# Kernel optimization log

Hardware: AMD Instinct MI355X
Metric: run time of the kernel (lower is better)

The kernel has to match this reference:

```python
import jax, jax.numpy as jnp
import numpy as np

B, N, D = 32, 2048, 128
HALF = D // 2
DT = 0.01  # interval = [0.0, 0.01], euler solver -> single step of size 0.01


def setup_inputs() -> dict:
    key = jax.random.key(0)
    ks = jax.random.split(key, 10)
    x = jax.random.normal(ks[0], (B, N, D), dtype=jnp.float32)
    hz = jax.random.normal(ks[1], (B, N, D), dtype=jnp.float32)
    # row-normalized random adjacency so adj @ h stays O(1) (avoids tanh saturation)
    adj = jax.random.uniform(ks[2], (N, N), dtype=jnp.float32) / N
    W1 = jax.random.normal(ks[3], (D, D), dtype=jnp.float32) * 0.05
    W2 = jax.random.normal(ks[4], (D, D), dtype=jnp.float32) * 0.05
    Wa = jax.random.normal(ks[5], (2 * D, 2 * D), dtype=jnp.float32) * 0.05
    ba = jnp.zeros((2 * D,), dtype=jnp.float32)
    Wb = jax.random.normal(ks[6], (2 * D, D), dtype=jnp.float32) * 0.05
    bb = jnp.zeros((D,), dtype=jnp.float32)
    # nn.Parameter init is zeros in torch; randomize in [0,0.1] for a nontrivial baseline
    eps = jax.random.uniform(ks[7], (B, N, HALF), dtype=jnp.float32) * 0.1
    return {"x": x, "hz": hz, "adj": adj, "W1": W1, "W2": W2,
            "Wa": Wa, "ba": ba, "Wb": Wb, "bb": bb, "eps": eps}


def reference(x, hz, adj, W1, W2, Wa, ba, Wb, bb, eps):
    # MLP gating: Linear(2D,2D) -> ReLU -> Linear(2D,D) -> Tanh
    u = jnp.concatenate([x, hz], axis=-1)            # [B,N,2D]
    h = jnp.tanh(jax.nn.relu(u @ Wa + ba) @ Wb + bb)  # [B,N,D]

    def gnn_func(h, W):
        # f(t, h) = tanh(A @ h @ W)  (graph diffusion ODE func)
        return jnp.tanh(jnp.einsum('nm,bmd->bnd', adj, h) @ W)

    def euler_step(h, W):
        # odeint(euler, t=[0, 0.01]): one step y1 = y0 + dt * f(0, y0)
        return h + DT * gnn_func(h, W)

    eps_c = jnp.clip(eps, 0.0, 0.1)
    for _ in range(2):
        h_f = euler_step(h, W1)[..., :HALF]                      # [B,N,D/2]
        h = jnp.concatenate([h_f, h[..., HALF:]], axis=-1)       # [B,N,D]
        h_s = eps_c * euler_step(h, W2)[..., HALF:]              # [B,N,D/2]
        h = jnp.concatenate([h_f, h_s], axis=-1)                 # [B,N,D]
    return h
```

## Files before the change

### kernel.cpp

```cpp
#include <hip/hip_runtime.h>


typedef unsigned short u16;
typedef unsigned int   u32;
typedef unsigned long long u64;
typedef __attribute__((ext_vector_type(8))) short bf8;
typedef __attribute__((ext_vector_type(4))) float f4;

#define AS1 __attribute__((address_space(1)))
#define AS3 __attribute__((address_space(3)))

__device__ __forceinline__ void gl_lds16(const void* g, void* l) {
  __builtin_amdgcn_global_load_lds((const AS1 u32*)g, (AS3 u32*)l, 16, 0, 0);
}
__device__ __forceinline__ float bf2f(u16 v) {
  u32 u = ((u32)v) << 16; return __builtin_bit_cast(float, u);
}
__device__ __forceinline__ u16 f2bf(float f) {
  u32 u = __builtin_bit_cast(u32, f);
  return (u16)((u + 0x7fffu + ((u >> 16) & 1u)) >> 16);
}
__device__ __forceinline__ float ldf(const void* p, size_t i, u32 isf32) {
  return isf32 ? ((const float*)p)[i] : bf2f(((const u16*)p)[i]);
}

__device__ __forceinline__ void stage128x32(const u16* grow0, int stride, u16* lds,
                                            int wave, int lane) {
  int r0 = wave * 16 + (lane >> 2);
  int c0 = (lane & 3) * 8;
  gl_lds16(grow0 + (size_t)r0 * stride + c0, lds + wave * 512);
  gl_lds16(grow0 + (size_t)(64 + r0) * stride + c0, lds + 2048 + wave * 512);
}
__device__ __forceinline__ void stage64x32(const u16* grow0, int stride, u16* lds,
                                           int wave, int lane) {
  gl_lds16(grow0 + (size_t)(wave * 16 + (lane >> 2)) * stride + (lane & 3) * 8,
           lds + wave * 512);
}

__global__ void detect_dtype(const u16* __restrict__ x_raw, u32* __restrict__ flag) {
  __shared__ int s;
  int tid = threadIdx.x;
  if (tid == 0) s = 0;
  __syncthreads();
  int huge = 0;
#pragma unroll
  for (int j = 0; j < 16; ++j) {
    u16 v = x_raw[tid * 16 + j];
    u32 e = (v >> 7) & 0xFF;
    if (e >= 0xC0) huge = 1;
  }
  if (huge) atomicOr(&s, 1);
  __syncthreads();
  if (tid == 0) flag[0] = (u32)s;
}

__global__ void cvt_bf16(const void* __restrict__ in, u16* __restrict__ out,
                         long in_off, int n, const u32* __restrict__ flag) {
  u32 isf32 = flag[0];
  int gid = blockIdx.x * 256 + threadIdx.x;
  long i = in_off + (long)gid * 4;
  if (gid * 4 >= n) return;
  u16 o0, o1, o2, o3;
  if (isf32) {
    f4 v = *(const f4*)&((const float*)in)[i];
    o0 = f2bf(v[0]); o1 = f2bf(v[1]); o2 = f2bf(v[2]); o3 = f2bf(v[3]);
  } else {
    u64 v = *(const u64*)&((const u16*)in)[i];
    o0 = (u16)v; o1 = (u16)(v >> 16); o2 = (u16)(v >> 32); o3 = (u16)(v >> 48);
  }
  u64 pk = (u64)o0 | ((u64)o1 << 16) | ((u64)o2 << 32) | ((u64)o3 << 48);
  *(u64*)&out[(size_t)gid * 4] = pk;
}

__global__ void prep_weights(const void* __restrict__ Wa, const void* __restrict__ Wb,
                             const void* __restrict__ W1, const void* __restrict__ W2,
                             u16* __restrict__ WaT, u16* __restrict__ WbT,
                             u16* __restrict__ W1T, u16* __restrict__ W2T,
                             const u32* __restrict__ flag) {
  u32 isf32 = flag[0];
  int i = blockIdx.x * 256 + threadIdx.x;
  if (i < 65536) {
    int o = i >> 8, k = i & 255; WaT[o * 256 + k] = f2bf(ldf(Wa, (size_t)k * 256 + o, isf32));
  } else if (i < 98304) {
    int j = i - 65536; int o = j >> 8, k = j & 255;
    WbT[o * 256 + k] = f2bf(ldf(Wb, (size_t)k * 128 + o, isf32));
  } else if (i < 106496) {
    int j = i - 98304; int jj = j >> 7, k = j & 127;
    W1T[jj * 128 + k] = f2bf(ldf(W1, (size_t)k * 128 + jj, isf32));
  } else {
    int j = i - 106496; int jj = j >> 7, k = j & 127;
    W2T[jj * 128 + k] = f2bf(ldf(W2, (size_t)k * 128 + 64 + jj, isf32));
  }
}

__global__ __launch_bounds__(256, 2) void mlp_fused(const void* __restrict__ x,
                                                    const void* __restrict__ hz,
                                                    const u16* __restrict__ WaT,
                                                    const void* __restrict__ ba,
                                                    const u16* __restrict__ WbT,
                                                    const void* __restrict__ bb,
                                                    const u16* __restrict__ W1T,
                                                    u16* __restrict__ hT,
                                                    u16* __restrict__ hW,
                                                    const u32* __restrict__ flag) {
  __shared__ __align__(16) u16 Z[64 * 264];
  __shared__ __align__(16) u16 pool[10240];
  u16* lA = pool;
  u16* lB = pool + 2048;
  u16* hN = pool;
  u32 isf32 = flag[0];
  int tid = threadIdx.x, lane = tid & 63, wave = tid >> 6;
  int col = lane & 15, quad = lane >> 4;
  int r0 = blockIdx.x * 64;
  int b = r0 >> 11;

  f4 acc[4][4] = {};
  for (int kk = 0; kk < 8; ++kk) {
    int k0 = kk * 32;
    const void* src = (kk < 4) ? x : hz;
    int csrc = (kk < 4) ? k0 : (k0 - 128);
    __syncthreads();
    {
      int row = tid >> 2, c0 = (tid & 3) * 8;
      size_t g = (size_t)(r0 + row) * 128 + csrc + c0;
      uint4 pk;
      if (isf32) {
        f4 v0 = *(const f4*)&((const float*)src)[g];
        f4 v1 = *(const f4*)&((const float*)src)[g + 4];
        pk.x = (u32)f2bf(v0[0]) | ((u32)f2bf(v0[1]) << 16);
        pk.y = (u32)f2bf(v0[2]) | ((u32)f2bf(v0[3]) << 16);
        pk.z = (u32)f2bf(v1[0]) | ((u32)f2bf(v1[1]) << 16);
        pk.w = (u32)f2bf(v1[2]) | ((u32)f2bf(v1[3]) << 16);
      } else {
        pk = *(const uint4*)&((const u16*)src)[g];
      }
      *(uint4*)&lA[row * 32 + c0] = pk;
    }
    stage128x32(WaT + k0, 256, lB, wave, lane);
    stage128x32(WaT + (size_t)128 * 256 + k0, 256, lB + 4096, wave, lane);
    __syncthreads();
    bf8 af[4], bfr[4];
#pragma unroll
    for (int mi = 0; mi < 4; ++mi) af[mi] = *(const bf8*)&lA[(mi * 16 + col) * 32 + quad * 8];
#pragma unroll
    for (int nj = 0; nj < 4; ++nj) bfr[nj] = *(const bf8*)&lB[(wave * 64 + nj * 16 + col) * 32 + quad * 8];
#pragma unroll
    for (int mi = 0; mi < 4; ++mi)
#pragma unroll
      for (int nj = 0; nj < 4; ++nj)
        acc[mi][nj] = __builtin_amdgcn_mfma_f32_16x16x32_bf16(af[mi], bfr[nj], acc[mi][nj], 0, 0, 0);
  }
#pragma unroll
  for (int mi = 0; mi < 4; ++mi)
#pragma unroll
    for (int nj = 0; nj < 4; ++nj) {
      int o = wave * 64 + nj * 16 + col;
      float bav = ldf(ba, o, isf32);
      int rl = mi * 16 + quad * 4;
#pragma unroll
      for (int r = 0; r < 4; ++r)
        Z[(rl + r) * 264 + o] = f2bf(fmaxf(acc[mi][nj][r] + bav, 0.f));
    }
  __syncthreads();

  f4 acc2[4][2] = {};
  for (int kk = 0; kk < 8; ++kk) {
    int k0 = kk * 32;
    if (kk) __syncthreads();
    stage128x32(WbT + k0, 256, lB, wave, lane);
    __syncthreads();
    bf8 az[4], bw[2];
#pragma unroll
    for (int mi = 0; mi < 4; ++mi) az[mi] = *(const bf8*)&Z[(mi * 16 + col) * 264 + k0 + quad * 8];
#pragma unroll
    for (int nj = 0; nj < 2; ++nj) bw[nj] = *(const bf8*)&lB[(wave * 32 + nj * 16 + col) * 32 + quad * 8];
#pragma unroll
    for (int mi = 0; mi < 4; ++mi)
#pragma unroll
      for (int nj = 0; nj < 2; ++nj)
        acc2[mi][nj] = __builtin_amdgcn_mfma_f32_16x16x32_bf16(az[mi], bw[nj], acc2[mi][nj], 0, 0, 0);
  }
  __syncthreads();

#pragma unroll
  for (int mi = 0; mi < 4; ++mi)
#pragma unroll
    for (int nj = 0; nj < 2; ++nj) {
      int d = wave * 32 + nj * 16 + col;
      float bbv = ldf(bb, d, isf32);
      int rl = mi * 16 + quad * 4;
      int rabs = r0 + rl;
      int n = rabs & 2047;
      u16 p[4];
#pragma unroll
      for (int r = 0; r < 4; ++r) {
        p[r] = f2bf(tanhf(acc2[mi][nj][r] + bbv));
        hN[(rl + r) * 136 + d] = p[r];
      }
      u64 pk = (u64)p[0] | ((u64)p[1] << 16) | ((u64)p[2] << 32) | ((u64)p[3] << 48);
      *(u64*)&hT[(size_t)(b * 128 + d) * 2048 + n] = pk;
    }
  __syncthreads();

  f4 acc3[4] = {};
#pragma unroll
  for (int ks = 0; ks < 4; ++ks) {
    bf8 aw[4], bg;
#pragma unroll
    for (int mi = 0; mi < 4; ++mi)
      aw[mi] = *(const bf8*)&W1T[(size_t)(mi * 16 + col) * 128 + ks * 32 + quad * 8];
    bg = *(const bf8*)&hN[(wave * 16 + col) * 136 + ks * 32 + quad * 8];
#pragma unroll
    for (int mi = 0; mi < 4; ++mi)
      acc3[mi] = __builtin_amdgcn_mfma_f32_16x16x32_bf16(aw[mi], bg, acc3[mi], 0, 0, 0);
  }
#pragma unroll
  for (int mi = 0; mi < 4; ++mi) {
    int rloc = wave * 16 + col;
    int ng = (r0 & 2047) + rloc;
#pragma unroll
    for (int r = 0; r < 4; ++r) {
      int j = mi * 16 + quad * 4 + r;
      hW[(size_t)(b * 64 + j) * 2048 + ng] = f2bf(acc3[mi][r]);
    }
  }
}

__global__ __launch_bounds__(256, 2) void fused_step2(const u16* __restrict__ hin,
                                                      const u16* __restrict__ hWT,
                                                      const u16* __restrict__ adjb,
                                                      const u16* __restrict__ WnT,
                                                      const void* __restrict__ eps,
                                                      u16* __restrict__ hout,
                                                      u16* __restrict__ hWout,
                                                      int half, const u32* __restrict__ flag) {
  __shared__ __align__(16) u16 smem[24576];
  u16* lA = smem;
  u16* lB = smem + 8192;
  u16* gN = smem;
  u32 isf32 = flag[0];
  int tid = threadIdx.x, lane = tid & 63, wave = tid >> 6;
  int col = lane & 15, quad = lane >> 4;
  int b = blockIdx.y;
  int n0 = blockIdx.x * 128;

  const u16* Arow = hWT + (size_t)(b * 64) * 2048;
  const u16* Brow = adjb + (size_t)n0 * 2048;

  f4 acc[4][2] = {};
  for (int kk = 0; kk < 16; ++kk) {
    int k0 = kk * 128;
#pragma unroll
    for (int p = 0; p < 4; ++p) {
      stage64x32(Arow + k0 + p * 32, 2048, lA + p * 2048, wave, lane);
      stage128x32(Brow + k0 + p * 32, 2048, lB + p * 4096, wave, lane);
    }
    __syncthreads();
#pragma unroll
    for (int p = 0; p < 4; ++p) {
      bf8 af[4], bfr[2];
#pragma unroll
      for (int mi = 0; mi < 4; ++mi) af[mi] = *(const bf8*)&lA[p * 2048 + (mi * 16 + col) * 32 + quad * 8];
#pragma unroll
      for (int nj = 0; nj < 2; ++nj) bfr[nj] = *(const bf8*)&lB[p * 4096 + (wave * 32 + nj * 16 + col) * 32 + quad * 8];
#pragma unroll
      for (int mi = 0; mi < 4; ++mi)
#pragma unroll
        for (int nj = 0; nj < 2; ++nj)
          acc[mi][nj] = __builtin_amdgcn_mfma_f32_16x16x32_bf16(af[mi], bfr[nj], acc[mi][nj], 0, 0, 0);
    }
    __syncthreads();
  }

  bool has_eps = (eps != nullptr);
  bool mk_hw = (WnT != nullptr);
  int dBase = half * 64;
#pragma unroll
  for (int mi = 0; mi < 4; ++mi)
#pragma unroll
    for (int nj = 0; nj < 2; ++nj) {
      int j0 = mi * 16 + quad * 4;
      int nl = wave * 32 + nj * 16 + col;
      int n = n0 + nl;
      float ev[4];
      if (has_eps) {
        size_t eoff = ((size_t)b * 2048 + n) * 64 + j0;
        if (isf32) {
          f4 e = *(const f4*)&((const float*)eps)[eoff];
          ev[0] = e[0]; ev[1] = e[1]; ev[2] = e[2]; ev[3] = e[3];
        } else {
          u64 e = *(const u64*)&((const u16*)eps)[eoff];
          ev[0] = bf2f((u16)e); ev[1] = bf2f((u16)(e >> 16));
          ev[2] = bf2f((u16)(e >> 32)); ev[3] = bf2f((u16)(e >> 48));
        }
      }
      u16 pv[4];
#pragma unroll
      for (int r = 0; r < 4; ++r) {
        int j = j0 + r;
        size_t idx = (size_t)(b * 128 + dBase + j) * 2048 + n;
        float hold = bf2f(hin[idx]);
        float nh = hold + 0.01f * tanhf(acc[mi][nj][r]);
        if (has_eps) {
          float e = fminf(fmaxf(ev[r], 0.f), 0.1f);
          nh = e * nh;
        }
        pv[r] = f2bf(nh);
        hout[idx] = pv[r];
      }
      if (mk_hw) {
        u64 pk = (u64)pv[0] | ((u64)pv[1] << 16) | ((u64)pv[2] << 32) | ((u64)pv[3] << 48);
        *(u64*)&gN[nl * 136 + dBase + j0] = pk;
      }
    }

  {
    int oh = (1 - half) * 64;
    const u16* src = hin + (size_t)(b * 128 + oh) * 2048 + n0;
    u16* dst = hout + (size_t)(b * 128 + oh) * 2048 + n0;
#pragma unroll
    for (int i = 0; i < 4; ++i) {
      int idx = i * 256 + tid;
      int rr = idx >> 4;
      int cc = (idx & 15) * 8;
      uint4 v = *(const uint4*)&src[(size_t)rr * 2048 + cc];
      *(uint4*)&dst[(size_t)rr * 2048 + cc] = v;
      if (mk_hw) {
        u16 t[8];
        *(uint4*)t = v;
#pragma unroll
        for (int q = 0; q < 8; ++q) gN[(cc + q) * 136 + oh + rr] = t[q];
      }
    }
  }

  if (mk_hw) {
    __syncthreads();
    f4 acc2[4][2] = {};
#pragma unroll
    for (int ks = 0; ks < 4; ++ks) {
      bf8 aw[4], bg[2];
#pragma unroll
      for (int mi = 0; mi < 4; ++mi)
        aw[mi] = *(const bf8*)&WnT[(size_t)(mi * 16 + col) * 128 + ks * 32 + quad * 8];
#pragma unroll
      for (int nj = 0; nj < 2; ++nj)
        bg[nj] = *(const bf8*)&gN[(wave * 32 + nj * 16 + col) * 136 + ks * 32 + quad * 8];
#pragma unroll
      for (int mi = 0; mi < 4; ++mi)
#pragma unroll
        for (int nj = 0; nj < 2; ++nj)
          acc2[mi][nj] = __builtin_amdgcn_mfma_f32_16x16x32_bf16(aw[mi], bg[nj], acc2[mi][nj], 0, 0, 0);
    }
#pragma unroll
    for (int mi = 0; mi < 4; ++mi)
#pragma unroll
      for (int nj = 0; nj < 2; ++nj) {
        int jp0 = mi * 16 + quad * 4;
        int n = n0 + wave * 32 + nj * 16 + col;
#pragma unroll
        for (int r = 0; r < 4; ++r)
          hWout[(size_t)(b * 64 + jp0 + r) * 2048 + n] = f2bf(acc2[mi][nj][r]);
      }
  }
}

__global__ void untranspose(const u16* __restrict__ hT, void* __restrict__ out,
                            const u32* __restrict__ flag) {
  __shared__ __align__(16) u16 t[64][65];
  u32 isf32 = flag[0];
  int b = blockIdx.z, d0 = blockIdx.y * 64, n0 = blockIdx.x * 64;
  int tid = threadIdx.x;
#pragma unroll
  for (int i = 0; i < 16; ++i) {
    int idx = tid + i * 256;
    int r = idx >> 6, c = idx & 63;
    t[r][c] = hT[(size_t)(b * 128 + d0 + r) * 2048 + n0 + c];
  }
  __syncthreads();
#pragma unroll
  for (int i = 0; i < 16; ++i) {
    int idx = tid + i * 256;
    int r = idx >> 6, c = idx & 63;
    size_t o = (size_t)(b * 2048 + n0 + r) * 128 + d0 + c;
    if (isf32) ((float*)out)[o] = bf2f(t[c][r]);
    else       ((u16*)out)[o] = t[c][r];
  }
}

extern "C" void kernel_launch(void* const* d_in, const int* in_sizes, int n_in,
                              void* d_out, int out_size, void* d_ws, size_t ws_size,
                              hipStream_t stream) {
  const void* x   = d_in[0];
  const void* hz  = d_in[1];
  const void* adj = d_in[2];
  const void* W1  = d_in[3];
  const void* W2  = d_in[4];
  const void* Wa  = d_in[5];
  const void* ba  = d_in[6];
  const void* Wb  = d_in[7];
  const void* bb  = d_in[8];
  const void* eps = d_in[9];

  char* ws = (char*)d_ws;
  u16* hA   = (u16*)(ws);
  u16* adjb = (u16*)(ws + (17ull << 20));
  u16* hWa  = (u16*)(ws + (26ull << 20));
  u16* hWb  = (u16*)(ws + (35ull << 20));
  u16* WaT  = (u16*)(ws + (44ull << 20));
  u16* WbT  = WaT + 256 * 256;
  u16* W1T  = WbT + 128 * 256;
  u16* W2T  = W1T + 64 * 128;
  u32* flag = (u32*)(W2T + 64 * 128);
  u16* hB   = (u16*)d_out;

  detect_dtype<<<dim3(1), dim3(256), 0, stream>>>((const u16*)x, flag);
  prep_weights<<<dim3(448), dim3(256), 0, stream>>>(Wa, Wb, W1, W2, WaT, WbT, W1T, W2T, flag);
  cvt_bf16<<<dim3(4096), dim3(256), 0, stream>>>(adj, adjb, 0, 4194304, flag);
  mlp_fused<<<dim3(1024), dim3(256), 0, stream>>>(x, hz, WaT, ba, WbT, bb, W1T, hA, hWa, flag);
  fused_step2<<<dim3(16, 32), dim3(256), 0, stream>>>(hA, hWa, adjb, W2T, nullptr, hB, hWb, 0, flag);
  fused_step2<<<dim3(16, 32), dim3(256), 0, stream>>>(hB, hWb, adjb, W1T, eps, hA, hWa, 1, flag);
  fused_step2<<<dim3(16, 32), dim3(256), 0, stream>>>(hA, hWa, adjb, W2T, nullptr, hB, hWb, 0, flag);
  fused_step2<<<dim3(16, 32), dim3(256), 0, stream>>>(hB, hWb, adjb, nullptr, eps, hA, nullptr, 1, flag);
  untranspose<<<dim3(32, 2, 32), dim3(256), 0, stream>>>(hA, d_out, flag);
}
```

Before: 348.2 us.

## Use FP8 adjacency and hW operands with fp8 MFMA in diffusion GEMM

```diff
diff --git a/kernel.cpp b/kernel.cpp
--- a/kernel.cpp
+++ b/kernel.cpp
@@ -2,6 +2,7 @@
 
 
 typedef unsigned short u16;
+typedef unsigned char  u8;
 typedef unsigned int   u32;
 typedef unsigned long long u64;
 typedef __attribute__((ext_vector_type(8))) short bf8;
@@ -19,6 +20,26 @@
 __device__ __forceinline__ u16 f2bf(float f) {
   u32 u = __builtin_bit_cast(u32, f);
   return (u16)((u + 0x7fffu + ((u >> 16) & 1u)) >> 16);
+}
+__device__ __forceinline__ u8 f2fp8(float f) {
+  u32 u = __builtin_bit_cast(u32, f);
+  u32 s = (u >> 24) & 0x80u;
+  int e = (int)((u >> 23) & 0xFFu) - 127;
+  u32 m = u & 0x7FFFFFu;
+  if (e > 8 || (e == 8 && m >= 0x700000u)) return (u8)(s | 0x7Eu);
+  if (e >= -6) {
+    u32 keep = m >> 20, rest = m & 0xFFFFFu;
+    keep += (rest > 0x80000u || (rest == 0x80000u && (keep & 1u))) ? 1u : 0u;
+    u32 v = ((u32)(e + 7) << 3) + keep;
+    if (v >= 0x7Fu) v = 0x7Eu;
+    return (u8)(s | v);
+  }
+  if (e < -10) return (u8)s;
+  u32 mm = 0x800000u | m;
+  int sh = 14 - e;
+  u32 q = mm >> sh, rem = mm & ((1u << sh) - 1u), half = 1u << (sh - 1);
+  q += (rem > half || (rem == half && (q & 1u))) ? 1u : 0u;
+  return (u8)(s | q);
 }
 __device__ __forceinline__ float ldf(const void* p, size_t i, u32 isf32) {
   return isf32 ? ((const float*)p)[i] : bf2f(((const u16*)p)[i]);
@@ -31,11 +52,6 @@
   gl_lds16(grow0 + (size_t)r0 * stride + c0, lds + wave * 512);
   gl_lds16(grow0 + (size_t)(64 + r0) * stride + c0, lds + 2048 + wave * 512);
 }
-__device__ __forceinline__ void stage64x32(const u16* grow0, int stride, u16* lds,
-                                           int wave, int lane) {
-  gl_lds16(grow0 + (size_t)(wave * 16 + (lane >> 2)) * stride + (lane & 3) * 8,
-           lds + wave * 512);
-}
 
 __global__ void detect_dtype(const u16* __restrict__ x_raw, u32* __restrict__ flag) {
   __shared__ int s;
@@ -54,22 +70,17 @@
   if (tid == 0) flag[0] = (u32)s;
 }
 
-__global__ void cvt_bf16(const void* __restrict__ in, u16* __restrict__ out,
-                         long in_off, int n, const u32* __restrict__ flag) {
+__global__ void cvt_fp8(const void* __restrict__ in, u8* __restrict__ out,
+                        int n, const u32* __restrict__ flag) {
   u32 isf32 = flag[0];
   int gid = blockIdx.x * 256 + threadIdx.x;
-  long i = in_off + (long)gid * 4;
   if (gid * 4 >= n) return;
-  u16 o0, o1, o2, o3;
-  if (isf32) {
-    f4 v = *(const f4*)&((const float*)in)[i];
-    o0 = f2bf(v[0]); o1 = f2bf(v[1]); o2 = f2bf(v[2]); o3 = f2bf(v[3]);
-  } else {
-    u64 v = *(const u64*)&((const u16*)in)[i];
-    o0 = (u16)v; o1 = (u16)(v >> 16); o2 = (u16)(v >> 32); o3 = (u16)(v >> 48);
-  }
-  u64 pk = (u64)o0 | ((u64)o1 << 16) | ((u64)o2 << 32) | ((u64)o3 << 48);
-  *(u64*)&out[(size_t)gid * 4] = pk;
+  size_t i = (size_t)gid * 4;
+  u32 pk = 0;
+#pragma unroll
+  for (int j = 0; j < 4; ++j)
+    pk |= (u32)f2fp8(ldf(in, i + j, isf32) * 65536.0f) << (8 * j);
+  *(u32*)&out[i] = pk;
 }
 
 __global__ void prep_weights(const void* __restrict__ Wa, const void* __restrict__ Wb,
@@ -101,7 +112,7 @@
                                                     const void* __restrict__ bb,
                                                     const u16* __restrict__ W1T,
                                                     u16* __restrict__ hT,
-                                                    u16* __restrict__ hW,
+                                                    u8* __restrict__ hW,
                                                     const u32* __restrict__ flag) {
   __shared__ __align__(16) u16 Z[64 * 264];
   __shared__ __align__(16) u16 pool[10240];
@@ -221,22 +232,22 @@
 #pragma unroll
     for (int r = 0; r < 4; ++r) {
       int j = mi * 16 + quad * 4 + r;
-      hW[(size_t)(b * 64 + j) * 2048 + ng] = f2bf(acc3[mi][r]);
+      hW[(size_t)(b * 64 + j) * 2048 + ng] = f2fp8(acc3[mi][r]);
     }
   }
 }
 
 __global__ __launch_bounds__(256, 2) void fused_step2(const u16* __restrict__ hin,
-                                                      const u16* __restrict__ hWT,
-                                                      const u16* __restrict__ adjb,
+                                                      const u8* __restrict__ hW8,
+                                                      const u8* __restrict__ adj8,
                                                       const u16* __restrict__ WnT,
                                                       const void* __restrict__ eps,
                                                       u16* __restrict__ hout,
-                                                      u16* __restrict__ hWout,
+                                                      u8* __restrict__ hWout,
                                                       int half, const u32* __restrict__ flag) {
   __shared__ __align__(16) u16 smem[24576];
-  u16* lA = smem;
-  u16* lB = smem + 8192;
+  u8* lA8 = (u8*)smem;
+  u8* lB8 = lA8 + 16384;
   u16* gN = smem;
   u32 isf32 = flag[0];
   int tid = threadIdx.x, lane = tid & 63, wave = tid >> 6;
@@ -244,30 +255,42 @@
   int b = blockIdx.y;
   int n0 = blockIdx.x * 128;
 
-  const u16* Arow = hWT + (size_t)(b * 64) * 2048;
-  const u16* Brow = adjb + (size_t)n0 * 2048;
+  const u8* Arow = hW8 + (size_t)(b * 64) * 2048;
+  const u8* Brow = adj8 + (size_t)n0 * 2048;
+  int r32 = lane & 31, kh16 = (lane >> 5) * 16;
+  int baseQ = (quad >> 1) * 512 + (quad & 1) * 8 + col * 16;
 
   f4 acc[4][2] = {};
-  for (int kk = 0; kk < 16; ++kk) {
-    int k0 = kk * 128;
-#pragma unroll
-    for (int p = 0; p < 4; ++p) {
-      stage64x32(Arow + k0 + p * 32, 2048, lA + p * 2048, wave, lane);
-      stage128x32(Brow + k0 + p * 32, 2048, lB + p * 4096, wave, lane);
-    }
-    __syncthreads();
-#pragma unroll
-    for (int p = 0; p < 4; ++p) {
-      bf8 af[4], bfr[2];
-#pragma unroll
-      for (int mi = 0; mi < 4; ++mi) af[mi] = *(const bf8*)&lA[p * 2048 + (mi * 16 + col) * 32 + quad * 8];
-#pragma unroll
-      for (int nj = 0; nj < 2; ++nj) bfr[nj] = *(const bf8*)&lB[p * 4096 + (wave * 32 + nj * 16 + col) * 32 + quad * 8];
+#pragma unroll 1
+  for (int t = 0; t < 8; ++t) {
+    {
+      int ga = wave >> 1, kca0 = (wave & 1) * 4;
+#pragma unroll
+      for (int q = 0; q < 4; ++q) {
+        int kc = kca0 + q;
+        gl_lds16(Arow + (size_t)(ga * 32 + r32) * 2048 + t * 256 + kc * 32 + kh16,
+                 lA8 + (ga * 8 + kc) * 1024);
+      }
+#pragma unroll
+      for (int kc = 0; kc < 8; ++kc)
+        gl_lds16(Brow + (size_t)(wave * 32 + r32) * 2048 + t * 256 + kc * 32 + kh16,
+                 lB8 + (wave * 8 + kc) * 1024);
+    }
+    __syncthreads();
+#pragma unroll
+    for (int ks = 0; ks < 8; ++ks) {
+      long long af[4], bfr[2];
 #pragma unroll
       for (int mi = 0; mi < 4; ++mi)
+        af[mi] = *(const long long*)&lA8[((mi >> 1) * 8 + ks) * 1024 + (mi & 1) * 256 + baseQ];
+#pragma unroll
+      for (int nj = 0; nj < 2; ++nj)
+        bfr[nj] = *(const long long*)&lB8[(wave * 8 + ks) * 1024 + nj * 256 + baseQ];
+#pragma unroll
+      for (int mi = 0; mi < 4; ++mi)
 #pragma unroll
         for (int nj = 0; nj < 2; ++nj)
-          acc[mi][nj] = __builtin_amdgcn_mfma_f32_16x16x32_bf16(af[mi], bfr[nj], acc[mi][nj], 0, 0, 0);
+          acc[mi][nj] = __builtin_amdgcn_mfma_f32_16x16x32_fp8_fp8(af[mi], bfr[nj], acc[mi][nj], 0, 0, 0);
     }
     __syncthreads();
   }
@@ -275,6 +298,7 @@
   bool has_eps = (eps != nullptr);
   bool mk_hw = (WnT != nullptr);
   int dBase = half * 64;
+  const float INV = 1.52587890625e-05f;
 #pragma unroll
   for (int mi = 0; mi < 4; ++mi)
 #pragma unroll
@@ -300,7 +324,7 @@
         int j = j0 + r;
         size_t idx = (size_t)(b * 128 + dBase + j) * 2048 + n;
         float hold = bf2f(hin[idx]);
-        float nh = hold + 0.01f * tanhf(acc[mi][nj][r]);
+        float nh = hold + 0.01f * tanhf(acc[mi][nj][r] * INV);
         if (has_eps) {
           float e = fminf(fmaxf(ev[r], 0.f), 0.1f);
           nh = e * nh;
@@ -360,7 +384,7 @@
         int n = n0 + wave * 32 + nj * 16 + col;
 #pragma unroll
         for (int r = 0; r < 4; ++r)
-          hWout[(size_t)(b * 64 + jp0 + r) * 2048 + n] = f2bf(acc2[mi][nj][r]);
+          hWout[(size_t)(b * 64 + jp0 + r) * 2048 + n] = f2fp8(acc2[mi][nj][r]);
       }
   }
 }
@@ -404,9 +428,9 @@
 
   char* ws = (char*)d_ws;
   u16* hA   = (u16*)(ws);
-  u16* adjb = (u16*)(ws + (17ull << 20));
-  u16* hWa  = (u16*)(ws + (26ull << 20));
-  u16* hWb  = (u16*)(ws + (35ull << 20));
+  u8*  adj8 = (u8*)(ws + (17ull << 20));
+  u8*  hWa  = (u8*)(ws + (26ull << 20));
+  u8*  hWb  = (u8*)(ws + (35ull << 20));
   u16* WaT  = (u16*)(ws + (44ull << 20));
   u16* WbT  = WaT + 256 * 256;
   u16* W1T  = WbT + 128 * 256;
@@ -416,11 +440,11 @@
 
   detect_dtype<<<dim3(1), dim3(256), 0, stream>>>((const u16*)x, flag);
   prep_weights<<<dim3(448), dim3(256), 0, stream>>>(Wa, Wb, W1, W2, WaT, WbT, W1T, W2T, flag);
-  cvt_bf16<<<dim3(4096), dim3(256), 0, stream>>>(adj, adjb, 0, 4194304, flag);
+  cvt_fp8<<<dim3(4096), dim3(256), 0, stream>>>(adj, adj8, 4194304, flag);
   mlp_fused<<<dim3(1024), dim3(256), 0, stream>>>(x, hz, WaT, ba, WbT, bb, W1T, hA, hWa, flag);
-  fused_step2<<<dim3(16, 32), dim3(256), 0, stream>>>(hA, hWa, adjb, W2T, nullptr, hB, hWb, 0, flag);
-  fused_step2<<<dim3(16, 32), dim3(256), 0, stream>>>(hB, hWb, adjb, W1T, eps, hA, hWa, 1, flag);
-  fused_step2<<<dim3(16, 32), dim3(256), 0, stream>>>(hA, hWa, adjb, W2T, nullptr, hB, hWb, 0, flag);
-  fused_step2<<<dim3(16, 32), dim3(256), 0, stream>>>(hB, hWb, adjb, nullptr, eps, hA, nullptr, 1, flag);
+  fused_step2<<<dim3(16, 32), dim3(256), 0, stream>>>(hA, hWa, adj8, W2T, nullptr, hB, hWb, 0, flag);
+  fused_step2<<<dim3(16, 32), dim3(256), 0, stream>>>(hB, hWb, adj8, W1T, eps, hA, hWa, 1, flag);
+  fused_step2<<<dim3(16, 32), dim3(256), 0, stream>>>(hA, hWa, adj8, W2T, nullptr, hB, hWb, 0, flag);
+  fused_step2<<<dim3(16, 32), dim3(256), 0, stream>>>(hB, hWb, adj8, nullptr, eps, hA, nullptr, 1, flag);
   untranspose<<<dim3(32, 2, 32), dim3(256), 0, stream>>>(hA, d_out, flag);
 }
```

New measurement: 372.9 us. 1.07x slower.
